# Kernel optimization log

Hardware: AMD Instinct MI355X
Metric: run time of the kernel (lower is better)

The kernel has to match this reference:

```python
import jax, jax.numpy as jnp
import numpy as np
from jax import lax

B, DIM, H, W = 16, 256, 64, 64
NH, KD = 8, 16
NH_KD = NH * KD        # 128
DH = 2 * NH_KD         # 256 (attn_ratio=2)
SCALE = KD ** -0.5
PE_LEN = 16


def conv1x1(x, Wt, b):
    # x: [B,Cin,H,W], Wt: [Cout,Cin]
    return jnp.einsum('oi,bihw->bohw', Wt, x) + b[None, :, None, None]


def dwconv3x3(x, Wt, b):
    # depthwise 3x3, pad 1. Wt: [C,1,3,3]
    C = x.shape[1]
    y = lax.conv_general_dilated(x, Wt, window_strides=(1, 1),
                                 padding=((1, 1), (1, 1)),
                                 feature_group_count=C,
                                 dimension_numbers=('NCHW', 'OIHW', 'NCHW'))
    return y + b[None, :, None, None]


def relu6(x):
    return jnp.clip(x, 0.0, 6.0)


def h_sigmoid(x):
    return jnp.clip(x + 3.0, 0.0, 6.0) / 6.0


def interp_linear(pe, N):
    # F.interpolate(mode='linear', align_corners=False). pe: [1,C,S] -> [1,C,N]
    S = pe.shape[-1]
    src = (jnp.arange(N, dtype=jnp.float32) + 0.5) * (S / N) - 0.5
    src = jnp.clip(src, 0.0, S - 1.0)
    lo = jnp.floor(src).astype(jnp.int32)
    hi = jnp.minimum(lo + 1, S - 1)
    w = (src - lo.astype(jnp.float32))[None, None, :]
    return pe[..., lo] * (1.0 - w) + pe[..., hi] * w


def axial_attn(qm, km, vm, pe_q, pe_k, N):
    # qm,km: [B,NH_KD,N] squeezed q/k means; vm: [B,DH,N]
    qn = (qm + interp_linear(pe_q, N)).reshape(B, NH, KD, N).transpose(0, 1, 3, 2)  # [B,h,N,kd]
    kn = (km + interp_linear(pe_k, N)).reshape(B, NH, KD, N)                        # [B,h,kd,N]
    vn = vm.reshape(B, NH, DH // NH, N).transpose(0, 1, 3, 2)                       # [B,h,N,d]
    attn = jax.nn.softmax(jnp.einsum('bhik,bhkj->bhij', qn, kn) * SCALE, axis=-1)
    xx = jnp.einsum('bhij,bhjd->bhid', attn, vn)                                    # [B,h,N,d]
    return xx.transpose(0, 1, 3, 2).reshape(B, DH, N)


def reference(x, Wq, bq, Wk, bk, Wv, bv, W_dw, b_dw, W_pw, b_pw,
              W_row, b_row, W_col, b_col, W_proj, b_proj,
              pe_rowq, pe_rowk, pe_colq, pe_colk):
    q = conv1x1(x, Wq, bq)   # [B,NH_KD,H,W]
    k = conv1x1(x, Wk, bk)   # [B,NH_KD,H,W]
    v = conv1x1(x, Wv, bv)   # [B,DH,H,W]

    qkv = jnp.concatenate([q, k, v], axis=1)        # [B,2*DH,H,W]
    qkv = relu6(dwconv3x3(qkv, W_dw, b_dw))
    qkv = conv1x1(qkv, W_pw, b_pw)                  # [B,DIM,H,W]

    # row attention (squeeze over W)
    xx_row = axial_attn(q.mean(-1), k.mean(-1), v.mean(-1), pe_rowq, pe_rowk, H)
    xx_row = conv1x1(relu6(xx_row[..., None]), W_row, b_row)          # [B,DH,H,1]

    # column attention (squeeze over H)
    xx_col = axial_attn(q.mean(-2), k.mean(-2), v.mean(-2), pe_colq, pe_colk, W)
    xx_col = conv1x1(relu6(xx_col[:, :, None, :]), W_col, b_col)      # [B,DH,1,W]

    xx = v + (xx_row + xx_col)                      # broadcast to [B,DH,H,W]
    xx = conv1x1(relu6(xx), W_proj, b_proj)         # [B,DIM,H,W]
    return h_sigmoid(xx) * qkv


def setup_inputs() -> dict:
    key = jax.random.key(0)
    ks = iter(jax.random.split(key, 32))

    def n(shape, fan_in=None):
        s = 1.0 if fan_in is None else 1.0 / np.sqrt(fan_in)
        return jax.random.normal(next(ks), shape, jnp.float32) * s

    return {
        'x': n((B, DIM, H, W)),
        'Wq': n((NH_KD, DIM), DIM), 'bq': n((NH_KD,), DIM),
        'Wk': n((NH_KD, DIM), DIM), 'bk': n((NH_KD,), DIM),
        'Wv': n((DH, DIM), DIM), 'bv': n((DH,), DIM),
        'W_dw': n((2 * DH, 1, 3, 3), 9), 'b_dw': n((2 * DH,), 9),
        'W_pw': n((DIM, 2 * DH), 2 * DH), 'b_pw': n((DIM,), 2 * DH),
        'W_row': n((DH, DH), DH), 'b_row': n((DH,), DH),
        'W_col': n((DH, DH), DH), 'b_col': n((DH,), DH),
        'W_proj': n((DIM, DH), DH), 'b_proj': n((DIM,), DH),
        'pe_rowq': n((1, NH_KD, PE_LEN)), 'pe_rowk': n((1, NH_KD, PE_LEN)),
        'pe_colq': n((1, NH_KD, PE_LEN)), 'pe_colk': n((1, NH_KD, PE_LEN)),
    }
```

## Files before the change

### kernel.cpp

```cpp
#include <hip/hip_runtime.h>


typedef short s16x8 __attribute__((ext_vector_type(8)));
typedef short s16x4 __attribute__((ext_vector_type(4)));
typedef float f32x4 __attribute__((ext_vector_type(4)));

#define OFF_QKVS 0ULL
#define OFF_DWO  67108864ULL
#define OFF_XBF  167772160ULL
#define OFF_MR   201326592ULL
#define OFF_MC   203423744ULL
#define OFF_XXA  205520896ULL
#define OFF_XRCT 207618048ULL
#define OFF_WQKV 209715200ULL
#define OFF_WPW  209977344ULL
#define OFF_WPR  210239488ULL
#define OFF_BQKV 210370560ULL

__device__ __forceinline__ float bf2f(unsigned short u) {
  unsigned int x = ((unsigned int)u) << 16;
  return __builtin_bit_cast(float, x);
}
__device__ __forceinline__ unsigned short f2bf(float f) {
  unsigned int x = __builtin_bit_cast(unsigned int, f);
  x += 0x7fffu + ((x >> 16) & 1u);
  return (unsigned short)(x >> 16);
}
__device__ __forceinline__ float relu6f(float v) { return fminf(fmaxf(v, 0.f), 6.f); }

__device__ __forceinline__ void mfma16(f32x4& d, s16x8 a, s16x8 b) {
  asm("v_mfma_f32_16x16x32_bf16 %0, %1, %2, %0" : "+v"(d) : "v"(a), "v"(b));
}

__global__ __launch_bounds__(256) void pack_k(
    const float* __restrict__ Wq, const float* __restrict__ Wk, const float* __restrict__ Wv,
    const float* __restrict__ bq, const float* __restrict__ bk, const float* __restrict__ bv,
    const float* __restrict__ Wpw, const float* __restrict__ Wpr,
    unsigned short* __restrict__ wqkv, unsigned short* __restrict__ wpw,
    unsigned short* __restrict__ wpr, float* __restrict__ bqkv)
{
  const int i = blockIdx.x * 256 + threadIdx.x;
  if (i < 131072) {
    const int o = i >> 8, k = i & 255;
    float v = (o < 128) ? Wq[o * 256 + k]
            : (o < 256) ? Wk[(o - 128) * 256 + k]
                        : Wv[(o - 256) * 256 + k];
    wqkv[i] = f2bf(v);
  } else if (i < 262144) {
    const int j = i - 131072;
    wpw[j] = f2bf(Wpw[j]);
  } else if (i < 327680) {
    const int j = i - 262144;
    wpr[j] = f2bf(Wpr[j]);
  } else if (i < 328192) {
    const int o = i - 327680;
    bqkv[o] = (o < 128) ? bq[o] : (o < 256) ? bk[o - 128] : bv[o - 256];
  }
}

__global__ __launch_bounds__(256) void xt_k(const float* __restrict__ x,
                                            unsigned short* __restrict__ xbf)
{
  __shared__ float tile[64][68];
  const int bid = blockIdx.x;
  const int nt = bid & 63, ct = (bid >> 6) & 3, b = bid >> 8;
  const int n0 = nt * 64, c0 = ct * 64;
  const int tid = threadIdx.x;
  #pragma unroll
  for (int p = 0; p < 4; ++p) {
    const int g = tid + p * 256;
    const int row = g >> 4, ch = g & 15;
    const float4 v = *(const float4*)&x[((size_t)b * 256 + c0 + row) * 4096 + n0 + ch * 4];
    *(float4*)&tile[row][ch * 4] = v;
  }
  __syncthreads();
  #pragma unroll
  for (int p = 0; p < 2; ++p) {
    const int g = tid + p * 256;
    const int nr = g >> 3, cc = g & 7;
    s16x8 o;
    #pragma unroll
    for (int q = 0; q < 8; ++q) o[q] = f2bf(tile[cc * 8 + q][nr]);
    *(s16x8*)&xbf[((size_t)b * 4096 + n0 + nr) * 256 + c0 + cc * 8] = o;
  }
}

template <int ROWS>
__device__ __forceinline__ void stage_rows(const unsigned short* __restrict__ src,
                                           int ld, unsigned short (*S)[72], int tid)
{
  #pragma unroll
  for (int p = 0; p < ROWS / 32; ++p) {
    const int g = tid + p * 256;
    const int r = g >> 3, sl = g & 7;
    *(s16x8*)&S[r][sl * 8] = *(const s16x8*)&src[(size_t)r * ld + sl * 8];
  }
}

__device__ __forceinline__ void compute64(const unsigned short (*As)[72],
                                          const unsigned short (*Xs)[72],
                                          f32x4 (*acc)[2], int wm, int wn, int lane)
{
  #pragma unroll
  for (int ks = 0; ks < 64; ks += 32) {
    s16x8 bF[2], aF[8];
    #pragma unroll
    for (int j = 0; j < 2; ++j)
      bF[j] = *(const s16x8*)&Xs[wn * 32 + j * 16 + (lane & 15)][ks + (lane >> 4) * 8];
    #pragma unroll
    for (int i = 0; i < 8; ++i)
      aF[i] = *(const s16x8*)&As[wm * 128 + i * 16 + (lane & 15)][ks + (lane >> 4) * 8];
    #pragma unroll
    for (int i = 0; i < 8; ++i)
      #pragma unroll
      for (int j = 0; j < 2; ++j)
        mfma16(acc[i][j], aF[i], bF[j]);
  }
}

__global__ __launch_bounds__(256, 2) void qkv_k(
    const unsigned short* __restrict__ wqkv, const float* __restrict__ bias,
    const unsigned short* __restrict__ xbf, unsigned short* __restrict__ qkvs,
    float* __restrict__ mr)
{
  __shared__ __align__(16) unsigned short As[256][72];
  __shared__ __align__(16) unsigned short Xs[64][72];
  __shared__ float msum[2][256];
  const int tid = threadIdx.x, lane = tid & 63, wave = tid >> 6;
  const int wm = wave >> 1, wn = wave & 1;
  const int bid = blockIdx.x;
  const int nt = bid & 63, mt = (bid >> 6) & 1, b = bid >> 7;
  const int row0 = mt * 256, col0 = nt * 64;

  f32x4 acc[8][2];
  #pragma unroll
  for (int i = 0; i < 8; ++i)
    #pragma unroll
    for (int j = 0; j < 2; ++j) acc[i][j] = (f32x4){0.f, 0.f, 0.f, 0.f};

  for (int k0 = 0; k0 < 256; k0 += 64) {
    stage_rows<256>(wqkv + (size_t)row0 * 256 + k0, 256, As, tid);
    stage_rows<64>(xbf + ((size_t)b * 4096 + col0) * 256 + k0, 256, Xs, tid);
    __syncthreads();
    compute64(As, Xs, acc, wm, wn, lane);
    __syncthreads();
  }

  #pragma unroll
  for (int i = 0; i < 8; ++i) {
    const int o0 = row0 + wm * 128 + i * 16 + ((lane >> 4) << 2);
    const float4 b4 = *(const float4*)&bias[o0];
    #pragma unroll
    for (int j = 0; j < 2; ++j) {
      const int n = col0 + wn * 32 + j * 16 + (lane & 15);
      s16x4 pk;
      pk[0] = f2bf(acc[i][j][0] + b4.x);
      pk[1] = f2bf(acc[i][j][1] + b4.y);
      pk[2] = f2bf(acc[i][j][2] + b4.z);
      pk[3] = f2bf(acc[i][j][3] + b4.w);
      *(s16x4*)&qkvs[((size_t)b * 4096 + n) * 512 + o0] = pk;
    }
    #pragma unroll
    for (int r = 0; r < 4; ++r) {
      float s = acc[i][0][r] + acc[i][1][r];
      s += __shfl_xor(s, 1);
      s += __shfl_xor(s, 2);
      s += __shfl_xor(s, 4);
      s += __shfl_xor(s, 8);
      if ((lane & 15) == 0)
        msum[wn][wm * 128 + i * 16 + ((lane >> 4) << 2) + r] = s;
    }
  }
  __syncthreads();
  mr[((size_t)b * 512 + row0 + tid) * 64 + nt] =
      (msum[0][tid] + msum[1][tid]) * (1.f / 64.f) + bias[row0 + tid];
}

__global__ __launch_bounds__(256) void mc_k(const unsigned short* __restrict__ qkvs,
                                            float* __restrict__ mc)
{
  const int bid = blockIdx.x;
  const int pos = bid & 63, b = bid >> 6;
  const int c = threadIdx.x * 2;
  float s0 = 0.f, s1 = 0.f;
  for (int t = 0; t < 64; ++t) {
    const int n = t * 64 + pos;
    const unsigned u = *(const unsigned*)&qkvs[((size_t)b * 4096 + n) * 512 + c];
    s0 += bf2f((unsigned short)u);
    s1 += bf2f((unsigned short)(u >> 16));
  }
  mc[((size_t)b * 512 + c) * 64 + pos] = s0 * (1.f / 64.f);
  mc[((size_t)b * 512 + c + 1) * 64 + pos] = s1 * (1.f / 64.f);
}

__global__ __launch_bounds__(512, 2) void dwm_k(
    const unsigned short* __restrict__ qkvs, const float* __restrict__ Wdw,
    const float* __restrict__ bdw, unsigned short* __restrict__ dwo)
{
  const int bid = blockIdx.x;
  const int h = bid & 63, b = bid >> 6;
  const int tid = threadIdx.x;
  const int c0 = (tid & 63) * 8;
  const int w0 = (tid >> 6) * 8;
  float w9[8][9], bs[8];
  #pragma unroll
  for (int q = 0; q < 8; ++q) {
    bs[q] = bdw[c0 + q];
    #pragma unroll
    for (int j = 0; j < 9; ++j) w9[q][j] = Wdw[(c0 + q) * 9 + j];
  }
  float acc[8][8];
  #pragma unroll
  for (int w = 0; w < 8; ++w)
    #pragma unroll
    for (int q = 0; q < 8; ++q) acc[w][q] = bs[q];

  const size_t base = (size_t)b * 4096 * 512;
  #pragma unroll
  for (int dr = 0; dr < 3; ++dr) {
    const int hh = h + dr - 1;
    if ((unsigned)hh < 64u) {
      s16x8 rowd[10];
      #pragma unroll
      for (int t = 0; t < 10; ++t) {
        const int ww = w0 + t - 1;
        if ((unsigned)ww < 64u)
          rowd[t] = *(const s16x8*)&qkvs[base + (size_t)(hh * 64 + ww) * 512 + c0];
        else
          rowd[t] = (s16x8){0, 0, 0, 0, 0, 0, 0, 0};
      }
      #pragma unroll
      for (int t = 0; t < 10; ++t) {
        float fv[8];
        #pragma unroll
        for (int q = 0; q < 8; ++q) fv[q] = bf2f((unsigned short)rowd[t][q]);
        #pragma unroll
        for (int dc = 0; dc < 3; ++dc) {
          const int w = t - dc;
          if (w >= 0 && w < 8) {
            #pragma unroll
            for (int q = 0; q < 8; ++q)
              acc[w][q] += w9[q][dr * 3 + dc] * fv[q];
          }
        }
      }
    }
  }
  #pragma unroll
  for (int w = 0; w < 8; ++w) {
    s16x8 o8;
    #pragma unroll
    for (int q = 0; q < 8; ++q) o8[q] = f2bf(relu6f(acc[w][q]));
    *(s16x8*)&dwo[base + (size_t)(h * 64 + w0 + w) * 512 + c0] = o8;
  }
}

__global__ __launch_bounds__(256, 2) void fin_k(
    const unsigned short* __restrict__ wpw, const float* __restrict__ bpw,
    const unsigned short* __restrict__ wpr, const float* __restrict__ bpr,
    const unsigned short* __restrict__ dwo, const unsigned short* __restrict__ qkvs,
    const float* __restrict__ xrct, float* __restrict__ out)
{
  __shared__ __align__(16) unsigned short As[256][72];
  __shared__ __align__(16) unsigned short Xs[64][72];
  const int tid = threadIdx.x, lane = tid & 63, wave = tid >> 6;
  const int wm = wave >> 1, wn = wave & 1;
  const int bid = blockIdx.x;
  const int nt = bid & 63, b = bid >> 6;
  const int col0 = nt * 64;

  f32x4 apw[8][2], apr[8][2];
  #pragma unroll
  for (int i = 0; i < 8; ++i)
    #pragma unroll
    for (int j = 0; j < 2; ++j) {
      apw[i][j] = (f32x4){0.f, 0.f, 0.f, 0.f};
      apr[i][j] = (f32x4){0.f, 0.f, 0.f, 0.f};
    }

  for (int k0 = 0; k0 < 512; k0 += 64) {
    stage_rows<256>(wpw + k0, 512, As, tid);
    stage_rows<64>(dwo + ((size_t)b * 4096 + col0) * 512 + k0, 512, Xs, tid);
    __syncthreads();
    compute64(As, Xs, apw, wm, wn, lane);
    __syncthreads();
  }
  const float* xr = &xrct[(((size_t)b * 2 + 0) * 64 + nt) * 256];
  const float* xc = &xrct[(((size_t)b * 2 + 1) * 64) * 256];
  for (int k0 = 0; k0 < 256; k0 += 64) {
    stage_rows<256>(wpr + k0, 256, As, tid);
    #pragma unroll
    for (int p = 0; p < 2; ++p) {
      const int g = tid + p * 256;
      const int r = g >> 3, sl = g & 7;
      const int kk = k0 + sl * 8;
      const s16x8 v = *(const s16x8*)&qkvs[((size_t)b * 4096 + col0 + r) * 512 + 256 + kk];
      const float4 a0 = *(const float4*)&xr[kk];
      const float4 a1 = *(const float4*)&xr[kk + 4];
      const float4 c0v = *(const float4*)&xc[(size_t)r * 256 + kk];
      const float4 c1v = *(const float4*)&xc[(size_t)r * 256 + kk + 4];
      const float ar[8] = {a0.x, a0.y, a0.z, a0.w, a1.x, a1.y, a1.z, a1.w};
      const float ac[8] = {c0v.x, c0v.y, c0v.z, c0v.w, c1v.x, c1v.y, c1v.z, c1v.w};
      s16x8 o;
      #pragma unroll
      for (int q = 0; q < 8; ++q)
        o[q] = f2bf(relu6f(bf2f((unsigned short)v[q]) + ar[q] + ac[q]));
      *(s16x8*)&Xs[r][sl * 8] = o;
    }
    __syncthreads();
    compute64(As, Xs, apr, wm, wn, lane);
    __syncthreads();
  }

  #pragma unroll
  for (int i = 0; i < 8; ++i) {
    const int o0 = wm * 128 + i * 16 + ((lane >> 4) << 2);
    const float4 bw = *(const float4*)&bpw[o0];
    const float4 bp = *(const float4*)&bpr[o0];
    const float bwv[4] = {bw.x, bw.y, bw.z, bw.w};
    const float bpv[4] = {bp.x, bp.y, bp.z, bp.w};
    #pragma unroll
    for (int j = 0; j < 2; ++j) {
      const int n = col0 + wn * 32 + j * 16 + (lane & 15);
      #pragma unroll
      for (int r = 0; r < 4; ++r) {
        const float hs = fminf(fmaxf(apr[i][j][r] + bpv[r] + 3.f, 0.f), 6.f) * (1.f / 6.f);
        out[((size_t)b * 256 + o0 + r) * 4096 + n] = hs * (apw[i][j][r] + bwv[r]);
      }
    }
  }
}

__global__ __launch_bounds__(256) void attn_k(
    const float* __restrict__ mr, const float* __restrict__ mc,
    const float* __restrict__ pe_rq, const float* __restrict__ pe_rk,
    const float* __restrict__ pe_cq, const float* __restrict__ pe_ck,
    float* __restrict__ xxa)
{
  __shared__ float qh[16][69], kh[16][69], vh[32][69], P[64][69];
  const int bid = blockIdx.x;
  const int hd = bid & 7, axis = (bid >> 3) & 1, b = bid >> 4;
  const float* m  = axis ? mc : mr;
  const float* pq = axis ? pe_cq : pe_rq;
  const float* pk = axis ? pe_ck : pe_rk;
  const int tid = threadIdx.x;

  #pragma unroll
  for (int p = 0; p < 4; ++p) {
    const int e = tid + p * 256;
    const int kd = e >> 6, i = e & 63;
    float srcp = 0.25f * (float)i - 0.375f;
    srcp = fminf(fmaxf(srcp, 0.f), 15.f);
    const int lo = (int)srcp;
    const int hi = min(lo + 1, 15);
    const float w = srcp - (float)lo;
    const int cq = hd * 16 + kd;
    qh[kd][i] = m[((size_t)b * 512 + cq) * 64 + i]
              + pq[cq * 16 + lo] * (1.f - w) + pq[cq * 16 + hi] * w;
    kh[kd][i] = m[((size_t)b * 512 + 128 + cq) * 64 + i]
              + pk[cq * 16 + lo] * (1.f - w) + pk[cq * 16 + hi] * w;
  }
  #pragma unroll
  for (int p = 0; p < 8; ++p) {
    const int e = tid + p * 256;
    const int d = e >> 6, j = e & 63;
    vh[d][j] = m[((size_t)b * 512 + 256 + hd * 32 + d) * 64 + j];
  }
  __syncthreads();
  {
    const int i = tid >> 2, j0 = (tid & 3) * 16;
    float qr[16];
    #pragma unroll
    for (int kd = 0; kd < 16; ++kd) qr[kd] = qh[kd][i];
    #pragma unroll
    for (int jj = 0; jj < 16; ++jj) {
      float s = 0.f;
      #pragma unroll
      for (int kd = 0; kd < 16; ++kd) s += qr[kd] * kh[kd][j0 + jj];
      P[i][j0 + jj] = s * 0.25f;
    }
  }
  __syncthreads();
  if (tid < 64) {
    float mx = -1e30f;
    for (int j = 0; j < 64; ++j) mx = fmaxf(mx, P[tid][j]);
    float sum = 0.f;
    for (int j = 0; j < 64; ++j) { const float e = __expf(P[tid][j] - mx); P[tid][j] = e; sum += e; }
    const float inv = 1.f / sum;
    for (int j = 0; j < 64; ++j) P[tid][j] *= inv;
  }
  __syncthreads();
  #pragma unroll
  for (int p = 0; p < 8; ++p) {
    const int e = tid + p * 256;
    const int d = e >> 6, i = e & 63;
    float s = 0.f;
    for (int j = 0; j < 64; ++j) s += P[i][j] * vh[d][j];
    xxa[(((size_t)(b * 2 + axis)) * 256 + hd * 32 + d) * 64 + i] = s;
  }
}

__global__ __launch_bounds__(256) void rc_k(
    const float* __restrict__ xxa, const float* __restrict__ Wrow, const float* __restrict__ brow,
    const float* __restrict__ Wcol, const float* __restrict__ bcol, float* __restrict__ xrct)
{
  __shared__ float stf[256][8];
  const int bid = blockIdx.x;
  const int ic = bid & 7, axis = (bid >> 3) & 1, b = bid >> 4;
  const float* W  = axis ? Wcol : Wrow;
  const float* bi = axis ? bcol : brow;
  const int tid = threadIdx.x;
  {
    const float* srcp = xxa + (((size_t)(b * 2 + axis)) * 256 + tid) * 64 + ic * 8;
    #pragma unroll
    for (int q = 0; q < 8; ++q) stf[tid][q] = relu6f(srcp[q]);
  }
  __syncthreads();
  float acc[8] = {0.f, 0.f, 0.f, 0.f, 0.f, 0.f, 0.f, 0.f};
  for (int c = 0; c < 256; ++c) {
    const float w = W[tid * 256 + c];
    const float4 s0 = *(const float4*)&stf[c][0];
    const float4 s1 = *(const float4*)&stf[c][4];
    acc[0] += w * s0.x; acc[1] += w * s0.y; acc[2] += w * s0.z; acc[3] += w * s0.w;
    acc[4] += w * s1.x; acc[5] += w * s1.y; acc[6] += w * s1.z; acc[7] += w * s1.w;
  }
  const float bb = bi[tid];
  #pragma unroll
  for (int q = 0; q < 8; ++q)
    xrct[(((size_t)(b * 2 + axis)) * 64 + ic * 8 + q) * 256 + tid] = acc[q] + bb;
}

extern "C" void kernel_launch(void* const* d_in, const int* in_sizes, int n_in,
                              void* d_out, int out_size, void* d_ws, size_t ws_size,
                              hipStream_t stream)
{
  const float* x    = (const float*)d_in[0];
  const float* Wq   = (const float*)d_in[1];
  const float* bq   = (const float*)d_in[2];
  const float* Wk   = (const float*)d_in[3];
  const float* bk   = (const float*)d_in[4];
  const float* Wv   = (const float*)d_in[5];
  const float* bv   = (const float*)d_in[6];
  const float* Wdw  = (const float*)d_in[7];
  const float* bdw  = (const float*)d_in[8];
  const float* Wpw  = (const float*)d_in[9];
  const float* bpw  = (const float*)d_in[10];
  const float* Wrow = (const float*)d_in[11];
  const float* brow = (const float*)d_in[12];
  const float* Wcol = (const float*)d_in[13];
  const float* bcol = (const float*)d_in[14];
  const float* Wpr  = (const float*)d_in[15];
  const float* bpr  = (const float*)d_in[16];
  const float* perq = (const float*)d_in[17];
  const float* perk = (const float*)d_in[18];
  const float* pecq = (const float*)d_in[19];
  const float* peck = (const float*)d_in[20];

  char* ws = (char*)d_ws;
  unsigned short* qkvs = (unsigned short*)(ws + OFF_QKVS);
  unsigned short* dwo  = (unsigned short*)(ws + OFF_DWO);
  unsigned short* xbf  = (unsigned short*)(ws + OFF_XBF);
  float* mr   = (float*)(ws + OFF_MR);
  float* mc   = (float*)(ws + OFF_MC);
  float* xxa  = (float*)(ws + OFF_XXA);
  float* xrct = (float*)(ws + OFF_XRCT);
  unsigned short* wqkv = (unsigned short*)(ws + OFF_WQKV);
  unsigned short* wpw  = (unsigned short*)(ws + OFF_WPW);
  unsigned short* wpr  = (unsigned short*)(ws + OFF_WPR);
  float* bqkv = (float*)(ws + OFF_BQKV);

  pack_k<<<1282, 256, 0, stream>>>(Wq, Wk, Wv, bq, bk, bv, Wpw, Wpr, wqkv, wpw, wpr, bqkv);
  xt_k<<<4096, 256, 0, stream>>>(x, xbf);

  qkv_k<<<2048, 256, 0, stream>>>(wqkv, bqkv, xbf, qkvs, mr);
  dwm_k<<<1024, 512, 0, stream>>>(qkvs, Wdw, bdw, dwo);
  mc_k<<<1024, 256, 0, stream>>>(qkvs, mc);
  attn_k<<<256, 256, 0, stream>>>(mr, mc, perq, perk, pecq, peck, xxa);
  rc_k<<<256, 256, 0, stream>>>(xxa, Wrow, brow, Wcol, bcol, xrct);
  fin_k<<<1024, 256, 0, stream>>>(wpw, bpw, wpr, bpr, dwo, qkvs, xrct, (float*)d_out);
}
```

Baseline: 216.2 us.

## Widen qkv and fin GEMM tiles to 128 columns with 512-thread blocks

Both GEMM kernels move from 256-thread blocks covering 64 spatial columns to 512-thread blocks covering 128 columns, with 8 waves laid out 2x4. Each staged weight tile in shared memory now serves twice as many columns, which halves the redundant weight loads per output. The row-mean and row/column broadcast index math is adjusted so one block spans two spatial rows. The trade-off is fewer blocks, more shared memory per block, and possibly lower occupancy under the (512,4) launch bound.

```diff
diff --git a/kernel.cpp b/kernel.cpp
--- a/kernel.cpp
+++ b/kernel.cpp
@@ -85,13 +85,13 @@
   }
 }
 
-template <int ROWS>
+template <int ROWS, int THREADS>
 __device__ __forceinline__ void stage_rows(const unsigned short* __restrict__ src,
                                            int ld, unsigned short (*S)[72], int tid)
 {
   #pragma unroll
-  for (int p = 0; p < ROWS / 32; ++p) {
-    const int g = tid + p * 256;
+  for (int p = 0; p < ROWS * 8 / THREADS; ++p) {
+    const int g = tid + p * THREADS;
     const int r = g >> 3, sl = g & 7;
     *(s16x8*)&S[r][sl * 8] = *(const s16x8*)&src[(size_t)r * ld + sl * 8];
   }
@@ -118,19 +118,19 @@
   }
 }
 
-__global__ __launch_bounds__(256, 2) void qkv_k(
+__global__ __launch_bounds__(512, 4) void qkv_k(
     const unsigned short* __restrict__ wqkv, const float* __restrict__ bias,
     const unsigned short* __restrict__ xbf, unsigned short* __restrict__ qkvs,
     float* __restrict__ mr)
 {
   __shared__ __align__(16) unsigned short As[256][72];
-  __shared__ __align__(16) unsigned short Xs[64][72];
-  __shared__ float msum[2][256];
+  __shared__ __align__(16) unsigned short Xs[128][72];
+  __shared__ float msum[4][256];
   const int tid = threadIdx.x, lane = tid & 63, wave = tid >> 6;
-  const int wm = wave >> 1, wn = wave & 1;
-  const int bid = blockIdx.x;
-  const int nt = bid & 63, mt = (bid >> 6) & 1, b = bid >> 7;
-  const int row0 = mt * 256, col0 = nt * 64;
+  const int wm = wave >> 2, wn = wave & 3;
+  const int bid = blockIdx.x;
+  const int nt = bid & 31, mt = (bid >> 5) & 1, b = bid >> 6;
+  const int row0 = mt * 256, col0 = nt * 128;
 
   f32x4 acc[8][2];
   #pragma unroll
@@ -139,8 +139,8 @@
     for (int j = 0; j < 2; ++j) acc[i][j] = (f32x4){0.f, 0.f, 0.f, 0.f};
 
   for (int k0 = 0; k0 < 256; k0 += 64) {
-    stage_rows<256>(wqkv + (size_t)row0 * 256 + k0, 256, As, tid);
-    stage_rows<64>(xbf + ((size_t)b * 4096 + col0) * 256 + k0, 256, Xs, tid);
+    stage_rows<256, 512>(wqkv + (size_t)row0 * 256 + k0, 256, As, tid);
+    stage_rows<128, 512>(xbf + ((size_t)b * 4096 + col0) * 256 + k0, 256, Xs, tid);
     __syncthreads();
     compute64(As, Xs, acc, wm, wn, lane);
     __syncthreads();
@@ -172,8 +172,11 @@
     }
   }
   __syncthreads();
-  mr[((size_t)b * 512 + row0 + tid) * 64 + nt] =
-      (msum[0][tid] + msum[1][tid]) * (1.f / 64.f) + bias[row0 + tid];
+  {
+    const int ol = tid & 255, hh = tid >> 8;
+    mr[((size_t)b * 512 + row0 + ol) * 64 + 2 * nt + hh] =
+        (msum[2 * hh][ol] + msum[2 * hh + 1][ol]) * (1.f / 64.f) + bias[row0 + ol];
+  }
 }
 
 __global__ __launch_bounds__(256) void mc_k(const unsigned short* __restrict__ qkvs,
@@ -255,19 +258,19 @@
   }
 }
 
-__global__ __launch_bounds__(256, 2) void fin_k(
+__global__ __launch_bounds__(512, 4) void fin_k(
     const unsigned short* __restrict__ wpw, const float* __restrict__ bpw,
     const unsigned short* __restrict__ wpr, const float* __restrict__ bpr,
     const unsigned short* __restrict__ dwo, const unsigned short* __restrict__ qkvs,
     const float* __restrict__ xrct, float* __restrict__ out)
 {
   __shared__ __align__(16) unsigned short As[256][72];
-  __shared__ __align__(16) unsigned short Xs[64][72];
+  __shared__ __align__(16) unsigned short Xs[128][72];
   const int tid = threadIdx.x, lane = tid & 63, wave = tid >> 6;
-  const int wm = wave >> 1, wn = wave & 1;
-  const int bid = blockIdx.x;
-  const int nt = bid & 63, b = bid >> 6;
-  const int col0 = nt * 64;
+  const int wm = wave >> 2, wn = wave & 3;
+  const int bid = blockIdx.x;
+  const int nt = bid & 31, b = bid >> 5;
+  const int col0 = nt * 128;
 
   f32x4 apw[8][2], apr[8][2];
   #pragma unroll
@@ -279,26 +282,27 @@
     }
 
   for (int k0 = 0; k0 < 512; k0 += 64) {
-    stage_rows<256>(wpw + k0, 512, As, tid);
-    stage_rows<64>(dwo + ((size_t)b * 4096 + col0) * 512 + k0, 512, Xs, tid);
+    stage_rows<256, 512>(wpw + k0, 512, As, tid);
+    stage_rows<128, 512>(dwo + ((size_t)b * 4096 + col0) * 512 + k0, 512, Xs, tid);
     __syncthreads();
     compute64(As, Xs, apw, wm, wn, lane);
     __syncthreads();
   }
-  const float* xr = &xrct[(((size_t)b * 2 + 0) * 64 + nt) * 256];
-  const float* xc = &xrct[(((size_t)b * 2 + 1) * 64) * 256];
+  const float* xrb = &xrct[(((size_t)b * 2 + 0) * 64) * 256];
+  const float* xcb = &xrct[(((size_t)b * 2 + 1) * 64) * 256];
   for (int k0 = 0; k0 < 256; k0 += 64) {
-    stage_rows<256>(wpr + k0, 256, As, tid);
+    stage_rows<256, 512>(wpr + k0, 256, As, tid);
     #pragma unroll
     for (int p = 0; p < 2; ++p) {
-      const int g = tid + p * 256;
+      const int g = tid + p * 512;
       const int r = g >> 3, sl = g & 7;
       const int kk = k0 + sl * 8;
+      const int hh = 2 * nt + (r >> 6), ww = r & 63;
       const s16x8 v = *(const s16x8*)&qkvs[((size_t)b * 4096 + col0 + r) * 512 + 256 + kk];
-      const float4 a0 = *(const float4*)&xr[kk];
-      const float4 a1 = *(const float4*)&xr[kk + 4];
-      const float4 c0v = *(const float4*)&xc[(size_t)r * 256 + kk];
-      const float4 c1v = *(const float4*)&xc[(size_t)r * 256 + kk + 4];
+      const float4 a0 = *(const float4*)&xrb[(size_t)hh * 256 + kk];
+      const float4 a1 = *(const float4*)&xrb[(size_t)hh * 256 + kk + 4];
+      const float4 c0v = *(const float4*)&xcb[(size_t)ww * 256 + kk];
+      const float4 c1v = *(const float4*)&xcb[(size_t)ww * 256 + kk + 4];
       const float ar[8] = {a0.x, a0.y, a0.z, a0.w, a1.x, a1.y, a1.z, a1.w};
       const float ac[8] = {c0v.x, c0v.y, c0v.z, c0v.w, c1v.x, c1v.y, c1v.z, c1v.w};
       s16x8 o;
@@ -472,10 +476,10 @@
   pack_k<<<1282, 256, 0, stream>>>(Wq, Wk, Wv, bq, bk, bv, Wpw, Wpr, wqkv, wpw, wpr, bqkv);
   xt_k<<<4096, 256, 0, stream>>>(x, xbf);
 
-  qkv_k<<<2048, 256, 0, stream>>>(wqkv, bqkv, xbf, qkvs, mr);
+  qkv_k<<<1024, 512, 0, stream>>>(wqkv, bqkv, xbf, qkvs, mr);
   dwm_k<<<1024, 512, 0, stream>>>(qkvs, Wdw, bdw, dwo);
   mc_k<<<1024, 256, 0, stream>>>(qkvs, mc);
   attn_k<<<256, 256, 0, stream>>>(mr, mc, perq, perk, pecq, peck, xxa);
   rc_k<<<256, 256, 0, stream>>>(xxa, Wrow, brow, Wcol, bcol, xrct);
-  fin_k<<<1024, 256, 0, stream>>>(wpw, bpw, wpr, bpr, dwo, qkvs, xrct, (float*)d_out);
-}
+  fin_k<<<512, 512, 0, stream>>>(wpw, bpw, wpr, bpr, dwo, qkvs, xrct, (float*)d_out);
+}
```

Measured after the change: 265.6 us. +22.9%, slower.

## Prefetch next K-tile into registers to overlap global loads with MFMA

Applied to the files above, without the earlier changes.

The QKV GEMM kernel and the fused pointwise/projection kernel now load the next K-slice of activations (and, in the QKV kernel, the weights) into registers before running the current tile's MFMA compute. The register copy is written to shared memory at the start of the next iteration. This is meant to hide global memory latency behind compute. In exchange it raises register pressure, most in qkv_k, where 8 extra s16x8 registers are held under launch_bounds(256,2), which could cause spills or lower occupancy.

```diff
diff --git a/kernel.cpp b/kernel.cpp
--- a/kernel.cpp
+++ b/kernel.cpp
@@ -132,16 +132,52 @@
   const int nt = bid & 63, mt = (bid >> 6) & 1, b = bid >> 7;
   const int row0 = mt * 256, col0 = nt * 64;
 
+  const unsigned short* Abase = wqkv + (size_t)row0 * 256;
+  const unsigned short* Xbase = xbf + ((size_t)b * 4096 + col0) * 256;
+
   f32x4 acc[8][2];
   #pragma unroll
   for (int i = 0; i < 8; ++i)
     #pragma unroll
     for (int j = 0; j < 2; ++j) acc[i][j] = (f32x4){0.f, 0.f, 0.f, 0.f};
 
+  s16x8 pA[8], pX[2];
+  #pragma unroll
+  for (int p = 0; p < 8; ++p) {
+    const int g = tid + p * 256, r = g >> 3, sl = g & 7;
+    pA[p] = *(const s16x8*)&Abase[(size_t)r * 256 + sl * 8];
+  }
+  #pragma unroll
+  for (int p = 0; p < 2; ++p) {
+    const int g = tid + p * 256, r = g >> 3, sl = g & 7;
+    pX[p] = *(const s16x8*)&Xbase[(size_t)r * 256 + sl * 8];
+  }
+
   for (int k0 = 0; k0 < 256; k0 += 64) {
-    stage_rows<256>(wqkv + (size_t)row0 * 256 + k0, 256, As, tid);
-    stage_rows<64>(xbf + ((size_t)b * 4096 + col0) * 256 + k0, 256, Xs, tid);
+    #pragma unroll
+    for (int p = 0; p < 8; ++p) {
+      const int g = tid + p * 256, r = g >> 3, sl = g & 7;
+      *(s16x8*)&As[r][sl * 8] = pA[p];
+    }
+    #pragma unroll
+    for (int p = 0; p < 2; ++p) {
+      const int g = tid + p * 256, r = g >> 3, sl = g & 7;
+      *(s16x8*)&Xs[r][sl * 8] = pX[p];
+    }
     __syncthreads();
+    if (k0 + 64 < 256) {
+      const int kn = k0 + 64;
+      #pragma unroll
+      for (int p = 0; p < 8; ++p) {
+        const int g = tid + p * 256, r = g >> 3, sl = g & 7;
+        pA[p] = *(const s16x8*)&Abase[(size_t)r * 256 + kn + sl * 8];
+      }
+      #pragma unroll
+      for (int p = 0; p < 2; ++p) {
+        const int g = tid + p * 256, r = g >> 3, sl = g & 7;
+        pX[p] = *(const s16x8*)&Xbase[(size_t)r * 256 + kn + sl * 8];
+      }
+    }
     compute64(As, Xs, acc, wm, wn, lane);
     __syncthreads();
   }
@@ -278,23 +314,48 @@
       apr[i][j] = (f32x4){0.f, 0.f, 0.f, 0.f};
     }
 
+  const unsigned short* Xb1 = dwo + ((size_t)b * 4096 + col0) * 512;
+  s16x8 pX[2];
+  #pragma unroll
+  for (int p = 0; p < 2; ++p) {
+    const int g = tid + p * 256, r = g >> 3, sl = g & 7;
+    pX[p] = *(const s16x8*)&Xb1[(size_t)r * 512 + sl * 8];
+  }
   for (int k0 = 0; k0 < 512; k0 += 64) {
     stage_rows<256>(wpw + k0, 512, As, tid);
-    stage_rows<64>(dwo + ((size_t)b * 4096 + col0) * 512 + k0, 512, Xs, tid);
+    #pragma unroll
+    for (int p = 0; p < 2; ++p) {
+      const int g = tid + p * 256, r = g >> 3, sl = g & 7;
+      *(s16x8*)&Xs[r][sl * 8] = pX[p];
+    }
     __syncthreads();
+    if (k0 + 64 < 512) {
+      const int kn = k0 + 64;
+      #pragma unroll
+      for (int p = 0; p < 2; ++p) {
+        const int g = tid + p * 256, r = g >> 3, sl = g & 7;
+        pX[p] = *(const s16x8*)&Xb1[(size_t)r * 512 + kn + sl * 8];
+      }
+    }
     compute64(As, Xs, apw, wm, wn, lane);
     __syncthreads();
   }
+
   const float* xr = &xrct[(((size_t)b * 2 + 0) * 64 + nt) * 256];
   const float* xc = &xrct[(((size_t)b * 2 + 1) * 64) * 256];
+  const unsigned short* Vb = qkvs + ((size_t)b * 4096 + col0) * 512 + 256;
+  s16x8 pV[2];
+  #pragma unroll
+  for (int p = 0; p < 2; ++p) {
+    const int g = tid + p * 256, r = g >> 3, sl = g & 7;
+    pV[p] = *(const s16x8*)&Vb[(size_t)r * 512 + sl * 8];
+  }
   for (int k0 = 0; k0 < 256; k0 += 64) {
     stage_rows<256>(wpr + k0, 256, As, tid);
     #pragma unroll
     for (int p = 0; p < 2; ++p) {
-      const int g = tid + p * 256;
-      const int r = g >> 3, sl = g & 7;
+      const int g = tid + p * 256, r = g >> 3, sl = g & 7;
       const int kk = k0 + sl * 8;
-      const s16x8 v = *(const s16x8*)&qkvs[((size_t)b * 4096 + col0 + r) * 512 + 256 + kk];
       const float4 a0 = *(const float4*)&xr[kk];
       const float4 a1 = *(const float4*)&xr[kk + 4];
       const float4 c0v = *(const float4*)&xc[(size_t)r * 256 + kk];
@@ -304,10 +365,18 @@
       s16x8 o;
       #pragma unroll
       for (int q = 0; q < 8; ++q)
-        o[q] = f2bf(relu6f(bf2f((unsigned short)v[q]) + ar[q] + ac[q]));
+        o[q] = f2bf(relu6f(bf2f((unsigned short)pV[p][q]) + ar[q] + ac[q]));
       *(s16x8*)&Xs[r][sl * 8] = o;
     }
     __syncthreads();
+    if (k0 + 64 < 256) {
+      const int kn = k0 + 64;
+      #pragma unroll
+      for (int p = 0; p < 2; ++p) {
+        const int g = tid + p * 256, r = g >> 3, sl = g & 7;
+        pV[p] = *(const s16x8*)&Vb[(size_t)r * 512 + kn + sl * 8];
+      }
+    }
     compute64(As, Xs, apr, wm, wn, lane);
     __syncthreads();
   }
```

Result: no change. 215.7 us (-0.2%).
